# Optimization experiments

Measured on AMD Instinct MI355X. Metric: run time of the kernel, lower is better.

The kernel has to match this reference:

```python
import jax, jax.numpy as jnp
import numpy as np

T = 8192          # sequence length
E = 1024          # embedding_dim
H = 1024          # hidden_dim
HD = H // 2       # per-direction hidden
K = 34            # tagset size
START, STOP = 32, 33
NEG = -10000.0


def setup_inputs() -> dict:
    key = jax.random.key(0)
    ks = jax.random.split(key, 16)
    s = 1.0 / np.sqrt(HD)  # torch LSTM/Linear init scale
    u = lambda k, shp, sc: jax.random.uniform(k, shp, jnp.float32, -sc, sc)
    inp = {
        "sentence": jax.random.normal(ks[0], (T, E), jnp.float32),
        "h0": jax.random.normal(ks[1], (2, HD), jnp.float32),
        "c0": jax.random.normal(ks[2], (2, HD), jnp.float32),
        "w_ih_f": u(ks[3], (4 * HD, E), s),
        "w_hh_f": u(ks[4], (4 * HD, HD), s),
        "b_ih_f": u(ks[5], (4 * HD,), s),
        "b_hh_f": u(ks[6], (4 * HD,), s),
        "w_ih_b": u(ks[7], (4 * HD, E), s),
        "w_hh_b": u(ks[8], (4 * HD, HD), s),
        "b_ih_b": u(ks[9], (4 * HD,), s),
        "b_hh_b": u(ks[10], (4 * HD,), s),
        "w_out": u(ks[11], (K, H), 1.0 / np.sqrt(H)),
        "b_out": u(ks[12], (K,), 1.0 / np.sqrt(H)),
    }
    trans = jax.random.normal(ks[13], (K, K), jnp.float32)
    trans = trans.at[START, :].set(NEG).at[:, STOP].set(NEG)
    inp["transitions"] = trans
    return inp


def _lstm_dir(x_proj, h0, c0, w_hh, reverse):
    # x_proj: [T, 4*HD] precomputed input projection (+ both biases)
    def step(carry, xp):
        h, c = carry
        g = xp + h @ w_hh.T
        i, f, gg, o = jnp.split(g, 4)
        i, f, o = jax.nn.sigmoid(i), jax.nn.sigmoid(f), jax.nn.sigmoid(o)
        c = f * c + i * jnp.tanh(gg)
        h = o * jnp.tanh(c)
        return (h, c), h
    _, hs = jax.lax.scan(step, (h0, c0), x_proj, reverse=reverse)
    return hs  # [T, HD]


def reference(sentence, h0, c0, w_ih_f, w_hh_f, b_ih_f, b_hh_f,
              w_ih_b, w_hh_b, b_ih_b, b_hh_b, w_out, b_out, transitions):
    # BiLSTM encoder (dropout is identity at inference)
    xp_f = sentence @ w_ih_f.T + (b_ih_f + b_hh_f)
    xp_b = sentence @ w_ih_b.T + (b_ih_b + b_hh_b)
    hs_f = _lstm_dir(xp_f, h0[0], c0[0], w_hh_f, reverse=False)
    hs_b = _lstm_dir(xp_b, h0[1], c0[1], w_hh_b, reverse=True)
    lstm_out = jnp.concatenate([hs_f, hs_b], axis=-1)        # [T, H]
    feats = lstm_out @ w_out.T + b_out                        # [T, K]

    # Viterbi decode: scores[next, prev] = fv[prev] + transitions[next, prev]
    fv0 = jnp.full((K,), NEG, jnp.float32).at[START].set(0.0)

    def vit_step(fv, feat):
        scores = fv[None, :] + transitions                    # [K, K]
        bp = jnp.argmax(scores, axis=1)                       # best prev per next
        fv_new = jnp.max(scores, axis=1) + feat
        return fv_new, bp

    fv, bps = jax.lax.scan(vit_step, fv0, feats)              # bps: [T, K]
    terminal = fv + transitions[STOP]
    best_last = jnp.argmax(terminal)
    path_score = terminal[best_last]

    def back_step(tag, bp_t):
        return bp_t[tag], tag

    _, best_path = jax.lax.scan(back_step, best_last, bps, reverse=True)  # [T]
    return path_score, best_path, sentence
```

## Files before the change

### kernel.cpp

```cpp
#include <hip/hip_runtime.h>
#include <hip/hip_bf16.h>

typedef float v4f __attribute__((ext_vector_type(4)));
typedef int   v4i __attribute__((ext_vector_type(4)));

#define T_LEN 8192
#define E_DIM 1024
#define HD    512
#define G4    2048
#define K_TAGS 34

#define XP_OFF      0ull
#define HS_OFF      134217728ull
#define FEATS_OFF   167772160ull
#define BP_OFF      168886272ull
#define BEST_OFF    169165824ull

#define BM 128
#define BN 128
#define BKK 16

__global__ __launch_bounds__(256) void xp_gemm(
    const float* __restrict__ A, const float* __restrict__ Wf, const float* __restrict__ Wb,
    const float* __restrict__ bihf, const float* __restrict__ bhhf,
    const float* __restrict__ bihb, const float* __restrict__ bhhb,
    float* __restrict__ xp)
{
  __shared__ __align__(16) float a_lds[BKK][BM + 4];
  __shared__ __align__(16) float b_lds[BKK][BN + 4];
  const int dir = blockIdx.z;
  const float* W   = dir ? Wb : Wf;
  const float* bih = dir ? bihb : bihf;
  const float* bhh = dir ? bhhb : bhhf;
  const int tid = threadIdx.x;
  const int srow = tid >> 1, sh = (tid & 1) * 8;
  const int tx = tid & 15, ty = tid >> 4;
  const size_t arow = (size_t)(blockIdx.x * BM + srow) * E_DIM;
  const size_t brow = (size_t)(blockIdx.y * BN + srow) * E_DIM;
  float acc[8][8];
  #pragma unroll
  for (int i = 0; i < 8; ++i)
    #pragma unroll
    for (int j = 0; j < 8; ++j) acc[i][j] = 0.f;

  for (int k0 = 0; k0 < E_DIM; k0 += BKK) {
    v4f a0 = *(const v4f*)(A + arow + k0 + sh);
    v4f a1 = *(const v4f*)(A + arow + k0 + sh + 4);
    v4f b0 = *(const v4f*)(W + brow + k0 + sh);
    v4f b1 = *(const v4f*)(W + brow + k0 + sh + 4);
    __syncthreads();
    #pragma unroll
    for (int j = 0; j < 4; ++j) {
      a_lds[sh + j][srow]     = a0[j];
      a_lds[sh + 4 + j][srow] = a1[j];
      b_lds[sh + j][srow]     = b0[j];
      b_lds[sh + 4 + j][srow] = b1[j];
    }
    __syncthreads();
    #pragma unroll
    for (int kk = 0; kk < BKK; ++kk) {
      v4f av0 = *(const v4f*)&a_lds[kk][ty * 8];
      v4f av1 = *(const v4f*)&a_lds[kk][ty * 8 + 4];
      v4f bv0 = *(const v4f*)&b_lds[kk][tx * 4];
      v4f bv1 = *(const v4f*)&b_lds[kk][64 + tx * 4];
      float av[8] = {av0[0],av0[1],av0[2],av0[3],av1[0],av1[1],av1[2],av1[3]};
      float bv[8] = {bv0[0],bv0[1],bv0[2],bv0[3],bv1[0],bv1[1],bv1[2],bv1[3]};
      #pragma unroll
      for (int i = 0; i < 8; ++i)
        #pragma unroll
        for (int j = 0; j < 8; ++j) acc[i][j] = fmaf(av[i], bv[j], acc[i][j]);
    }
  }
  const int gm  = blockIdx.x * BM + ty * 8;
  const int gnl = blockIdx.y * BN + tx * 4;
  const int gnh = gnl + 64;
  float bias[8];
  #pragma unroll
  for (int j = 0; j < 4; ++j) bias[j]     = bih[gnl + j] + bhh[gnl + j];
  #pragma unroll
  for (int j = 0; j < 4; ++j) bias[4 + j] = bih[gnh + j] + bhh[gnh + j];
  float* outp = xp + ((size_t)dir * T_LEN) * G4;
  #pragma unroll
  for (int i = 0; i < 8; ++i) {
    v4f o0 = {acc[i][0]+bias[0], acc[i][1]+bias[1], acc[i][2]+bias[2], acc[i][3]+bias[3]};
    v4f o1 = {acc[i][4]+bias[4], acc[i][5]+bias[5], acc[i][6]+bias[6], acc[i][7]+bias[7]};
    *(v4f*)(outp + (size_t)(gm + i) * G4 + gnl) = o0;
    *(v4f*)(outp + (size_t)(gm + i) * G4 + gnh) = o1;
  }
}

__device__ __forceinline__ float row16_sum(float x) {
  x += __int_as_float(__builtin_amdgcn_update_dpp(0, __float_as_int(x), 0x111, 0xf, 0xf, true));
  x += __int_as_float(__builtin_amdgcn_update_dpp(0, __float_as_int(x), 0x112, 0xf, 0xf, true));
  x += __int_as_float(__builtin_amdgcn_update_dpp(0, __float_as_int(x), 0x114, 0xf, 0xf, true));
  x += __int_as_float(__builtin_amdgcn_update_dpp(0, __float_as_int(x), 0x118, 0xf, 0xf, true));
  return x;
}

__device__ __forceinline__ float sigmoidf_(float x) { return 1.f / (1.f + expf(-x)); }

__global__ __launch_bounds__(1024) void lstm_kernel(
    const float* __restrict__ h0, const float* __restrict__ c0,
    const float* __restrict__ whhf, const float* __restrict__ whhb,
    const float* __restrict__ xp, float* __restrict__ hs)
{
  const int b = blockIdx.x;
  const int dir = b >> 5, bb = b & 31;
  const int tid = threadIdx.x;
  const int w = tid >> 6, L = tid & 63;
  const float* whh = dir ? whhb : whhf;
  const float* xpd = xp + (size_t)dir * T_LEN * G4;
  float* hsd = hs + (size_t)dir * T_LEN * HD;
  __shared__ __align__(16) float hl[HD];
  __shared__ __align__(16) float red2[16][4][4];
  __shared__ float xpl[2][64];

  float wreg[4][8];
  #pragma unroll
  for (int j = 0; j < 4; ++j) {
    int r = 4 * w + j;
    int grow = (r >> 4) * HD + bb * 16 + (r & 15);
    const float* p = whh + (size_t)grow * HD + 8 * L;
    v4f q0 = *(const v4f*)p;
    v4f q1 = *(const v4f*)(p + 4);
    #pragma unroll
    for (int kk = 0; kk < 4; ++kk) { wreg[j][kk] = q0[kk]; wreg[j][4 + kk] = q1[kk]; }
  }
  float cst = 0.f;
  if (w == 1 && L < 16) cst = c0[dir * HD + bb * 16 + L];
  const int xcol = (L >> 4) * HD + bb * 16 + (L & 15);
  if (w == 2) xpl[0][L] = xpd[(size_t)(dir ? (T_LEN - 1) : 0) * G4 + xcol];
  __syncthreads();

  for (int s = 0; s < T_LEN; ++s) {
    const int t = dir ? (T_LEN - 1 - s) : s;

    if (w == 0) {
      if (s == 0) {
        const float* hp = h0 + dir * HD + 8 * L;
        v4f a = *(const v4f*)hp;
        v4f bq = *(const v4f*)(hp + 4);
        *(v4f*)&hl[8 * L]     = a;
        *(v4f*)&hl[8 * L + 4] = bq;
      } else {
        const int tp = dir ? (t + 1) : (t - 1);
        const float* hp = hsd + (size_t)tp * HD + 8 * L;
        asm volatile("s_sleep 6" ::: "memory");
        v4i ia, ib;
        do {
          asm volatile("global_load_dwordx4 %0, %2, off sc0 sc1\n"
                       "global_load_dwordx4 %1, %2, off offset:16 sc0 sc1\n"
                       "s_waitcnt vmcnt(0)"
                       : "=&v"(ia), "=&v"(ib) : "v"(hp) : "memory");
        } while (((ia[0] == -1) | (ia[1] == -1) | (ia[2] == -1) | (ia[3] == -1) |
                  (ib[0] == -1) | (ib[1] == -1) | (ib[2] == -1) | (ib[3] == -1)) != 0);
        v4f fa, fb;
        #pragma unroll
        for (int kk = 0; kk < 4; ++kk) { fa[kk] = __int_as_float(ia[kk]); fb[kk] = __int_as_float(ib[kk]); }
        *(v4f*)&hl[8 * L]     = fa;
        *(v4f*)&hl[8 * L + 4] = fb;
      }
    }
    __syncthreads();

    v4f h0v = *(const v4f*)&hl[8 * L];
    v4f h1v = *(const v4f*)&hl[8 * L + 4];
    float hr[8] = {h0v[0], h0v[1], h0v[2], h0v[3], h1v[0], h1v[1], h1v[2], h1v[3]};
    float a4[4];
    #pragma unroll
    for (int j = 0; j < 4; ++j) {
      float a = 0.f;
      #pragma unroll
      for (int kk = 0; kk < 8; ++kk) a = fmaf(wreg[j][kk], hr[kk], a);
      a4[j] = row16_sum(a);
    }
    if ((L & 15) == 15) {
      int q = L >> 4;
      v4f rv = {a4[0], a4[1], a4[2], a4[3]};
      *(v4f*)&red2[w][q][0] = rv;
    }
    __syncthreads();

    if (w == 1) {
      const int u = L & 15;
      const int ww = L >> 2, j = L & 3;
      const float sum = red2[ww][0][j] + red2[ww][1][j] + red2[ww][2][j] + red2[ww][3][j]
                      + xpl[s & 1][L];
      const float gv = ((L >> 4) == 2) ? tanhf(sum) : sigmoidf_(sum);
      const float ig = __shfl(gv, u);
      const float fg = __shfl(gv, u + 16);
      const float gg = __shfl(gv, u + 32);
      const float og = __shfl(gv, u + 48);
      if (L < 16) {
        cst = fg * cst + ig * gg;
        const float hval = og * tanhf(cst);
        float* hp = hsd + (size_t)t * HD + bb * 16 + L;
        asm volatile("global_store_dword %0, %1, off sc0 sc1" :: "v"(hp), "v"(hval) : "memory");
      }
    } else if (w == 2 && s + 1 < T_LEN) {
      const int tn = dir ? (t - 1) : (t + 1);
      xpl[(s + 1) & 1][L] = xpd[(size_t)tn * G4 + xcol];
    }
  }
}

__global__ __launch_bounds__(256) void feats_kernel(
    const float* __restrict__ hs, const float* __restrict__ wout,
    const float* __restrict__ bout, float* __restrict__ feats)
{
  __shared__ __align__(16) float xs[32][132];
  __shared__ __align__(16) float wl[34][132];
  const int tid = threadIdx.x;
  const int t0 = blockIdx.x * 32;
  const int m = tid & 31, ng = tid >> 5;
  float acc[5] = {0.f, 0.f, 0.f, 0.f, 0.f};
  for (int cc = 0; cc < 8; ++cc) {
    const int d = cc >> 2;
    const int c0 = (cc & 3) * 128;
    const float* hsrc = hs + (size_t)d * T_LEN * HD;
    const int wcol = d * HD + c0;
    __syncthreads();
    {
      const int row = tid >> 3, seg = tid & 7;
      const float* src = hsrc + (size_t)(t0 + row) * HD + c0 + seg * 16;
      #pragma unroll
      for (int i = 0; i < 4; ++i) {
        v4f v = *(const v4f*)(src + i * 4);
        *(v4f*)&xs[row][seg * 16 + i * 4] = v;
      }
    }
    for (int i = tid; i < 34 * 32; i += 256) {
      const int r = i >> 5, q = i & 31;
      v4f v = *(const v4f*)(wout + (size_t)r * E_DIM + wcol + q * 4);
      *(v4f*)&wl[r][q * 4] = v;
    }
    __syncthreads();
    for (int kq = 0; kq < 32; ++kq) {
      v4f xv = *(const v4f*)&xs[m][kq * 4];
      #pragma unroll
      for (int sl = 0; sl < 5; ++sl) {
        const int n = ng + sl * 8;
        if (n < K_TAGS) {
          v4f wv = *(const v4f*)&wl[n][kq * 4];
          acc[sl] = fmaf(xv[0], wv[0], acc[sl]);
          acc[sl] = fmaf(xv[1], wv[1], acc[sl]);
          acc[sl] = fmaf(xv[2], wv[2], acc[sl]);
          acc[sl] = fmaf(xv[3], wv[3], acc[sl]);
        }
      }
    }
  }
  #pragma unroll
  for (int sl = 0; sl < 5; ++sl) {
    const int n = ng + sl * 8;
    if (n < K_TAGS) feats[(size_t)(t0 + m) * K_TAGS + n] = acc[sl] + bout[n];
  }
}

__global__ __launch_bounds__(64) void viterbi_kernel(
    const float* __restrict__ feats, const float* __restrict__ trans,
    float* __restrict__ d_out, int* __restrict__ bestlast, unsigned char* __restrict__ bp)
{
  const int L = threadIdx.x;
  const int n = (L < K_TAGS) ? L : 0;
  const bool act = (L < K_TAGS);
  float tr[K_TAGS];
  #pragma unroll
  for (int p = 0; p < K_TAGS; ++p) tr[p] = trans[n * K_TAGS + p];
  const float tstop = trans[33 * K_TAGS + n];
  __shared__ float fvs[K_TAGS];
  if (act) fvs[n] = (n == 32) ? 0.f : -10000.f;
  asm volatile("s_waitcnt lgkmcnt(0)" ::: "memory");
  __builtin_amdgcn_sched_barrier(0);

  float feat_next = feats[n];
  float fvreg = 0.f;
  for (int t = 0; t < T_LEN; ++t) {
    const float feat = feat_next;
    if (t + 1 < T_LEN) feat_next = feats[(size_t)(t + 1) * K_TAGS + n];
    float val[K_TAGS];
    int   idx[K_TAGS];
    #pragma unroll
    for (int p = 0; p < K_TAGS; ++p) { val[p] = fvs[p] + tr[p]; idx[p] = p; }
    #pragma unroll
    for (int st = 1; st < K_TAGS; st <<= 1) {
      #pragma unroll
      for (int i = 0; i + st < K_TAGS; i += 2 * st) {
        if (val[i + st] > val[i]) { val[i] = val[i + st]; idx[i] = idx[i + st]; }
      }
    }
    fvreg = val[0] + feat;
    if (act) {
      bp[(size_t)t * K_TAGS + n] = (unsigned char)idx[0];
      fvs[n] = fvreg;
    }
    asm volatile("s_waitcnt lgkmcnt(0)" ::: "memory");
    __builtin_amdgcn_sched_barrier(0);
  }
  if (act) fvs[n] = fvreg + tstop;
  asm volatile("s_waitcnt lgkmcnt(0)" ::: "memory");
  __builtin_amdgcn_sched_barrier(0);
  if (L == 0) {
    float best = -3.4e38f; int bi = 0;
    for (int k = 0; k < K_TAGS; ++k) {
      const float v = fvs[k];
      if (v > best) { best = v; bi = k; }
    }
    d_out[0] = best;
    *bestlast = bi;
  }
}

__global__ __launch_bounds__(1024) void backtrace_kernel(
    const unsigned char* __restrict__ bp, const int* __restrict__ bestlast,
    float* __restrict__ d_out)
{
  __shared__ unsigned char exitl[128 * K_TAGS];
  __shared__ unsigned char entl[128];
  const int tid = threadIdx.x;
  for (int W = tid; W < 128 * K_TAGS; W += 1024) {
    const int c = W / K_TAGS;
    int tg = W % K_TAGS;
    for (int t = c * 64 + 63; t >= c * 64; --t) tg = bp[(size_t)t * K_TAGS + tg];
    exitl[W] = (unsigned char)tg;
  }
  __syncthreads();
  if (tid == 0) {
    int tag = *bestlast;
    entl[127] = (unsigned char)tag;
    for (int c = 127; c >= 1; --c) {
      tag = exitl[c * K_TAGS + tag];
      entl[c - 1] = (unsigned char)tag;
    }
  }
  __syncthreads();
  if (tid < 128) {
    const int c = tid;
    int tg = entl[c];
    for (int t = c * 64 + 63; t >= c * 64; --t) {
      d_out[1 + t] = (float)tg;
      tg = bp[(size_t)t * K_TAGS + tg];
    }
  }
}

extern "C" void kernel_launch(void* const* d_in, const int* in_sizes, int n_in,
                              void* d_out, int out_size, void* d_ws, size_t ws_size,
                              hipStream_t stream)
{
  const float* sent = (const float*)d_in[0];
  const float* h0   = (const float*)d_in[1];
  const float* c0   = (const float*)d_in[2];
  const float* wihf = (const float*)d_in[3];
  const float* whhf = (const float*)d_in[4];
  const float* bihf = (const float*)d_in[5];
  const float* bhhf = (const float*)d_in[6];
  const float* wihb = (const float*)d_in[7];
  const float* whhb = (const float*)d_in[8];
  const float* bihb = (const float*)d_in[9];
  const float* bhhb = (const float*)d_in[10];
  const float* wout = (const float*)d_in[11];
  const float* bout = (const float*)d_in[12];
  const float* trans = (const float*)d_in[13];

  float* out = (float*)d_out;
  char* ws = (char*)d_ws;
  float* xp    = (float*)(ws + XP_OFF);
  float* hs    = (float*)(ws + HS_OFF);
  float* feats = (float*)(ws + FEATS_OFF);
  unsigned char* bp = (unsigned char*)(ws + BP_OFF);
  int* bestlast = (int*)(ws + BEST_OFF);

  hipMemsetAsync(hs, 0xFF, (size_t)2 * T_LEN * HD * sizeof(float), stream);

  hipMemcpyAsync(out + 1 + T_LEN, sent, (size_t)T_LEN * E_DIM * sizeof(float),
                 hipMemcpyDeviceToDevice, stream);

  dim3 g1(T_LEN / BM, G4 / BN, 2);
  xp_gemm<<<g1, 256, 0, stream>>>(sent, wihf, wihb, bihf, bhhf, bihb, bhhb, xp);

  lstm_kernel<<<64, 1024, 0, stream>>>(h0, c0, whhf, whhb, xp, hs);

  feats_kernel<<<T_LEN / 32, 256, 0, stream>>>(hs, wout, bout, feats);

  viterbi_kernel<<<1, 64, 0, stream>>>(feats, trans, out, bestlast, bp);

  backtrace_kernel<<<1, 1024, 0, stream>>>(bp, bestlast, out);
}
```

Baseline: 19.56 ms.

## Fuse input-projection GEMM with LSTM recurrence via sentinel-flagged streaming

```diff
diff --git a/kernel.cpp b/kernel.cpp
--- a/kernel.cpp
+++ b/kernel.cpp
@@ -16,27 +16,53 @@
 #define BP_OFF      168886272ull
 #define BEST_OFF    169165824ull
 
+#define SENT32 0xFFFFFFFFu
+
+__device__ __forceinline__ float xp_sent_ld(const float* p) {
+  unsigned u = *(const unsigned*)p;
+  while (u == SENT32) {
+    asm volatile("global_load_dword %0, %1, off sc0 sc1\ns_waitcnt vmcnt(0)"
+                 : "=v"(u) : "v"(p) : "memory");
+  }
+  return __uint_as_float(u);
+}
+
+__device__ __forceinline__ float row16_sum(float x) {
+  x += __int_as_float(__builtin_amdgcn_update_dpp(0, __float_as_int(x), 0x111, 0xf, 0xf, true));
+  x += __int_as_float(__builtin_amdgcn_update_dpp(0, __float_as_int(x), 0x112, 0xf, 0xf, true));
+  x += __int_as_float(__builtin_amdgcn_update_dpp(0, __float_as_int(x), 0x114, 0xf, 0xf, true));
+  x += __int_as_float(__builtin_amdgcn_update_dpp(0, __float_as_int(x), 0x118, 0xf, 0xf, true));
+  return x;
+}
+
+__device__ __forceinline__ float sigmoidf_(float x) { return 1.f / (1.f + expf(-x)); }
+
 #define BM 128
 #define BN 128
 #define BKK 16
 
-__global__ __launch_bounds__(256) void xp_gemm(
-    const float* __restrict__ A, const float* __restrict__ Wf, const float* __restrict__ Wb,
-    const float* __restrict__ bihf, const float* __restrict__ bhhf,
-    const float* __restrict__ bihb, const float* __restrict__ bhhb,
-    float* __restrict__ xp)
-{
-  __shared__ __align__(16) float a_lds[BKK][BM + 4];
-  __shared__ __align__(16) float b_lds[BKK][BN + 4];
-  const int dir = blockIdx.z;
+__device__ void gemm_role(int g, const float* A, const float* Wf, const float* Wb,
+    const float* bihf, const float* bhhf,
+    const float* bihb, const float* bhhb, float* xp)
+{
+  const int dir  = g & 1;
+  const int u    = g >> 1;
+  const int rank = u >> 2, nq = u & 3;
+  const int bx = dir ? (63 - rank) : rank;
+  const int quarter = threadIdx.x >> 8;
+  const int by = nq * 4 + quarter;
+  const int tid = threadIdx.x & 255;
+
+  __shared__ __align__(16) float a_lds[4][BKK][BM + 4];
+  __shared__ __align__(16) float b_lds[4][BKK][BN + 4];
+
   const float* W   = dir ? Wb : Wf;
   const float* bih = dir ? bihb : bihf;
   const float* bhh = dir ? bhhb : bhhf;
-  const int tid = threadIdx.x;
   const int srow = tid >> 1, sh = (tid & 1) * 8;
   const int tx = tid & 15, ty = tid >> 4;
-  const size_t arow = (size_t)(blockIdx.x * BM + srow) * E_DIM;
-  const size_t brow = (size_t)(blockIdx.y * BN + srow) * E_DIM;
+  const size_t arow = (size_t)(bx * BM + srow) * E_DIM;
+  const size_t brow = (size_t)(by * BN + srow) * E_DIM;
   float acc[8][8];
   #pragma unroll
   for (int i = 0; i < 8; ++i)
@@ -51,18 +77,18 @@
     __syncthreads();
     #pragma unroll
     for (int j = 0; j < 4; ++j) {
-      a_lds[sh + j][srow]     = a0[j];
-      a_lds[sh + 4 + j][srow] = a1[j];
-      b_lds[sh + j][srow]     = b0[j];
-      b_lds[sh + 4 + j][srow] = b1[j];
+      a_lds[quarter][sh + j][srow]     = a0[j];
+      a_lds[quarter][sh + 4 + j][srow] = a1[j];
+      b_lds[quarter][sh + j][srow]     = b0[j];
+      b_lds[quarter][sh + 4 + j][srow] = b1[j];
     }
     __syncthreads();
     #pragma unroll
     for (int kk = 0; kk < BKK; ++kk) {
-      v4f av0 = *(const v4f*)&a_lds[kk][ty * 8];
-      v4f av1 = *(const v4f*)&a_lds[kk][ty * 8 + 4];
-      v4f bv0 = *(const v4f*)&b_lds[kk][tx * 4];
-      v4f bv1 = *(const v4f*)&b_lds[kk][64 + tx * 4];
+      v4f av0 = *(const v4f*)&a_lds[quarter][kk][ty * 8];
+      v4f av1 = *(const v4f*)&a_lds[quarter][kk][ty * 8 + 4];
+      v4f bv0 = *(const v4f*)&b_lds[quarter][kk][tx * 4];
+      v4f bv1 = *(const v4f*)&b_lds[quarter][kk][64 + tx * 4];
       float av[8] = {av0[0],av0[1],av0[2],av0[3],av1[0],av1[1],av1[2],av1[3]};
       float bv[8] = {bv0[0],bv0[1],bv0[2],bv0[3],bv1[0],bv1[1],bv1[2],bv1[3]};
       #pragma unroll
@@ -71,8 +97,8 @@
         for (int j = 0; j < 8; ++j) acc[i][j] = fmaf(av[i], bv[j], acc[i][j]);
     }
   }
-  const int gm  = blockIdx.x * BM + ty * 8;
-  const int gnl = blockIdx.y * BN + tx * 4;
+  const int gm  = bx * BM + ty * 8;
+  const int gnl = by * BN + tx * 4;
   const int gnh = gnl + 64;
   float bias[8];
   #pragma unroll
@@ -84,27 +110,16 @@
   for (int i = 0; i < 8; ++i) {
     v4f o0 = {acc[i][0]+bias[0], acc[i][1]+bias[1], acc[i][2]+bias[2], acc[i][3]+bias[3]};
     v4f o1 = {acc[i][4]+bias[4], acc[i][5]+bias[5], acc[i][6]+bias[6], acc[i][7]+bias[7]};
-    *(v4f*)(outp + (size_t)(gm + i) * G4 + gnl) = o0;
-    *(v4f*)(outp + (size_t)(gm + i) * G4 + gnh) = o1;
-  }
-}
-
-__device__ __forceinline__ float row16_sum(float x) {
-  x += __int_as_float(__builtin_amdgcn_update_dpp(0, __float_as_int(x), 0x111, 0xf, 0xf, true));
-  x += __int_as_float(__builtin_amdgcn_update_dpp(0, __float_as_int(x), 0x112, 0xf, 0xf, true));
-  x += __int_as_float(__builtin_amdgcn_update_dpp(0, __float_as_int(x), 0x114, 0xf, 0xf, true));
-  x += __int_as_float(__builtin_amdgcn_update_dpp(0, __float_as_int(x), 0x118, 0xf, 0xf, true));
-  return x;
-}
-
-__device__ __forceinline__ float sigmoidf_(float x) { return 1.f / (1.f + expf(-x)); }
-
-__global__ __launch_bounds__(1024) void lstm_kernel(
-    const float* __restrict__ h0, const float* __restrict__ c0,
-    const float* __restrict__ whhf, const float* __restrict__ whhb,
-    const float* __restrict__ xp, float* __restrict__ hs)
-{
-  const int b = blockIdx.x;
+    float* p0 = outp + (size_t)(gm + i) * G4 + gnl;
+    float* p1 = outp + (size_t)(gm + i) * G4 + gnh;
+    asm volatile("global_store_dwordx4 %0, %1, off sc0 sc1" :: "v"(p0), "v"(o0) : "memory");
+    asm volatile("global_store_dwordx4 %0, %1, off sc0 sc1" :: "v"(p1), "v"(o1) : "memory");
+  }
+}
+
+__device__ void lstm_role(int b, const float* h0, const float* c0,
+    const float* whhf, const float* whhb, const float* xp, float* hs)
+{
   const int dir = b >> 5, bb = b & 31;
   const int tid = threadIdx.x;
   const int w = tid >> 6, L = tid & 63;
@@ -129,7 +144,7 @@
   float cst = 0.f;
   if (w == 1 && L < 16) cst = c0[dir * HD + bb * 16 + L];
   const int xcol = (L >> 4) * HD + bb * 16 + (L & 15);
-  if (w == 2) xpl[0][L] = xpd[(size_t)(dir ? (T_LEN - 1) : 0) * G4 + xcol];
+  if (w == 2) xpl[0][L] = xp_sent_ld(xpd + (size_t)(dir ? (T_LEN - 1) : 0) * G4 + xcol);
   __syncthreads();
 
   for (int s = 0; s < T_LEN; ++s) {
@@ -199,9 +214,23 @@
       }
     } else if (w == 2 && s + 1 < T_LEN) {
       const int tn = dir ? (t - 1) : (t + 1);
-      xpl[(s + 1) & 1][L] = xpd[(size_t)tn * G4 + xcol];
-    }
-  }
+      xpl[(s + 1) & 1][L] = xp_sent_ld(xpd + (size_t)tn * G4 + xcol);
+    }
+  }
+}
+
+__global__ __launch_bounds__(1024) void gemm_lstm_kernel(
+    const float* __restrict__ sent, const float* __restrict__ h0,
+    const float* __restrict__ c0,
+    const float* __restrict__ wihf, const float* __restrict__ whhf,
+    const float* __restrict__ bihf, const float* __restrict__ bhhf,
+    const float* __restrict__ wihb, const float* __restrict__ whhb,
+    const float* __restrict__ bihb, const float* __restrict__ bhhb,
+    float* __restrict__ xp, float* __restrict__ hs)
+{
+  const int b = blockIdx.x;
+  if (b < 64) lstm_role(b, h0, c0, whhf, whhb, xp, hs);
+  else        gemm_role(b - 64, sent, wihf, wihb, bihf, bhhf, bihb, bhhb, xp);
 }
 
 __global__ __launch_bounds__(256) void feats_kernel(
@@ -371,15 +400,14 @@
   unsigned char* bp = (unsigned char*)(ws + BP_OFF);
   int* bestlast = (int*)(ws + BEST_OFF);
 
+  hipMemsetAsync(xp, 0xFF, (size_t)2 * T_LEN * G4 * sizeof(float), stream);
   hipMemsetAsync(hs, 0xFF, (size_t)2 * T_LEN * HD * sizeof(float), stream);
 
   hipMemcpyAsync(out + 1 + T_LEN, sent, (size_t)T_LEN * E_DIM * sizeof(float),
                  hipMemcpyDeviceToDevice, stream);
 
-  dim3 g1(T_LEN / BM, G4 / BN, 2);
-  xp_gemm<<<g1, 256, 0, stream>>>(sent, wihf, wihb, bihf, bhhf, bihb, bhhb, xp);
-
-  lstm_kernel<<<64, 1024, 0, stream>>>(h0, c0, whhf, whhb, xp, hs);
+  gemm_lstm_kernel<<<576, 1024, 0, stream>>>(
+      sent, h0, c0, wihf, whhf, bihf, bhhf, wihb, whhb, bihb, bhhb, xp, hs);
 
   feats_kernel<<<T_LEN / 32, 256, 0, stream>>>(hs, wout, bout, feats);
 
```

Result: faster. 19.14 ms (-2.1%).
